# Kernel optimization log

Hardware: AMD Instinct MI355X
Metric: run time of the kernel (lower is better)

Reference implementation:

```python
import jax, jax.numpy as jnp
import numpy as np


def setup_inputs() -> dict:
    key = jax.random.key(0)
    kx, kr, kq, kk, kv = jax.random.split(key, 5)
    B, T, N, C = 4, 8, 2048, 128
    w_scale = 1.0 / np.sqrt(C)  # keep logits in a sane range
    return {
        "x": jax.random.normal(kx, (B, T, N, C), dtype=jnp.float32),
        "residual_source": jax.random.normal(kr, (B, N, C), dtype=jnp.float32),
        "Wq": jax.random.normal(kq, (C, C), dtype=jnp.float32) * w_scale,
        "Wk": jax.random.normal(kk, (C, C), dtype=jnp.float32) * w_scale,
        "Wv": jax.random.normal(kv, (C, C), dtype=jnp.float32) * w_scale,
    }


def reference(x, residual_source, Wq, Wk, Wv):
    # x: [B, T, N, C]; residual_source: [B, M, C] (expanded along T in the
    # original via unsqueeze+expand; here we exploit broadcasting instead of
    # materializing the [B, T, M, C] copy -- same math, k/v identical per T).
    q = jnp.einsum("btnc,cd->btnd", x, Wq)               # [B, T, N, D]
    k = jnp.einsum("bmc,cd->bmd", residual_source, Wk)   # [B, M, D]
    v = jnp.einsum("bmc,cd->bmd", residual_source, Wv)   # [B, M, D]
    # Unscaled attention, exactly as in the original (no 1/sqrt(d)).
    affinities = jnp.einsum("btnd,bmd->btnm", q, k)       # [B, T, N, M]
    attn = jax.nn.softmax(affinities, axis=-1)
    residual = jnp.einsum("btnm,bmd->btnd", attn, v)      # [B, T, N, D]
    return x + residual
```

## Files before the change

kernel.cpp:

```cpp
#include <hip/hip_runtime.h>


#define Bn 4
#define Tn 8
#define Nn 2048
#define Cn 128
#define Mn 2048
#define NTILES 32
#define QROWS 128
#define NQT (Nn / QROWS)

typedef __attribute__((ext_vector_type(4))) float f32x4;
typedef __attribute__((ext_vector_type(16))) float f32x16;
typedef __attribute__((ext_vector_type(8))) _Float16 f16x8;
typedef __attribute__((ext_vector_type(4))) unsigned int u32x4;
typedef __attribute__((address_space(3))) unsigned char lds_uc;
typedef const __attribute__((address_space(1))) unsigned char glb_uc;

__device__ __forceinline__ unsigned short f2h(float f) {
  _Float16 h = (_Float16)f;
  return __builtin_bit_cast(unsigned short, h);
}
__device__ __forceinline__ unsigned int pk2(float a, float b) {
  auto v = __builtin_amdgcn_cvt_pkrtz(a, b);
  return __builtin_bit_cast(unsigned int, v);
}
__device__ __forceinline__ f16x8 lds_read8w(const unsigned char* base, int row,
                                            int colByte) {
  int byte = row * 256 + (colByte ^ ((row & 15) << 4));
  return *(const f16x8*)(base + byte);
}
__device__ __forceinline__ f16x8 lds_read8v(const unsigned char* base, int row,
                                            int colByte) {
  int byte = row * 128 + (colByte ^ ((row & 7) << 4));
  return *(const f16x8*)(base + byte);
}
__device__ __forceinline__ void gld16(const void* g, void* l) {
  __builtin_amdgcn_global_load_lds((glb_uc*)g, (lds_uc*)l, 16, 0, 0);
}

#define MKPF(dst, sv, base)                                        \
  {                                                                \
    unsigned a0 = pk2(sv[base + 0], sv[base + 1]);                 \
    unsigned b0 = pk2(sv[base + 4], sv[base + 5]);                 \
    unsigned a1 = pk2(sv[base + 2], sv[base + 3]);                 \
    unsigned b1 = pk2(sv[base + 6], sv[base + 7]);                 \
    asm("v_permlane32_swap_b32 %0, %1" : "+v"(a0), "+v"(b0));      \
    asm("v_permlane32_swap_b32 %0, %1" : "+v"(a1), "+v"(b1));      \
    u32x4 tmp = {a0, a1, b0, b1};                                  \
    dst = __builtin_bit_cast(f16x8, tmp);                          \
  }

__global__ __launch_bounds__(256) void proj_kv_kernel(
    const float* __restrict__ rs, const float* __restrict__ Wk,
    const float* __restrict__ Wv, unsigned short* __restrict__ k_ws,
    unsigned short* __restrict__ vt_ws) {
  __shared__ unsigned char smem[48 * 1024];
  unsigned char* rsh = smem;
  unsigned char* wt = smem + 16 * 1024;

  const int bid = blockIdx.x;
  const int b = bid >> 5;
  const int kt = bid & 31;
  const int m0 = kt << 6;
  const int tid = threadIdx.x;
  const int wv = tid >> 6, lane = tid & 63;

  {
    const float4* g = (const float4*)(rs + ((size_t)b * Mn + m0) * Cn);
#pragma unroll
    for (int i = 0; i < 8; ++i) {
      int f = tid + i * 256;
      int row = f >> 5, c4 = f & 31;
      float4 v = g[f];
      int byte = row * 256 + ((c4 * 8) ^ ((row & 15) << 4));
      *(ushort4*)(rsh + byte) =
          make_ushort4(f2h(v.x), f2h(v.y), f2h(v.z), f2h(v.w));
    }
  }

#define STAGE_WT(Wp)                                                          \
  {                                                                           \
    const float4* g = (const float4*)(Wp);                                    \
    _Pragma("unroll") for (int i = 0; i < 16; ++i) {                          \
      int f = tid + i * 256;                                                  \
      int cc = f >> 5, d0 = (f & 31) * 4;                                     \
      float4 v = g[f];                                                        \
      float vv[4] = {v.x, v.y, v.z, v.w};                                     \
      _Pragma("unroll") for (int j = 0; j < 4; ++j) {                         \
        int row = d0 + j;                                                     \
        int byte = row * 256 + ((cc * 2) ^ ((row & 15) << 4));                \
        *(unsigned short*)(wt + byte) = f2h(vv[j]);                           \
      }                                                                       \
    }                                                                         \
  }

  STAGE_WT(Wk);
  __syncthreads();

  const int arow = wv * 16 + (lane & 15);
  f16x8 ah[4];
#pragma unroll
  for (int ks = 0; ks < 4; ++ks)
    ah[ks] = lds_read8w(rsh, arow, (lane >> 4) * 16 + ks * 64);

  f32x4 acc[8];
#pragma unroll
  for (int df = 0; df < 8; ++df) acc[df] = (f32x4)(0.0f);
#pragma unroll
  for (int ks = 0; ks < 4; ++ks)
#pragma unroll
    for (int df = 0; df < 8; ++df) {
      f16x8 bf = lds_read8w(wt, df * 16 + (lane & 15), (lane >> 4) * 16 + ks * 64);
      acc[df] = __builtin_amdgcn_mfma_f32_16x16x32_f16(ah[ks], bf, acc[df], 0, 0, 0);
    }
  {
    unsigned char* kb = (unsigned char*)k_ws + ((size_t)b * NTILES + kt) * 16384;
#pragma unroll
    for (int df = 0; df < 8; ++df)
#pragma unroll
      for (int r = 0; r < 4; ++r) {
        int row = wv * 16 + (lane >> 4) * 4 + r;
        int dcol = df * 16 + (lane & 15);
        int byte = row * 256 + ((dcol * 2) ^ ((row & 15) << 4));
        *(unsigned short*)(kb + byte) = f2h(acc[df][r]);
      }
  }
  __syncthreads();

  STAGE_WT(Wv);
  __syncthreads();
#pragma unroll
  for (int df = 0; df < 8; ++df) acc[df] = (f32x4)(0.0f);
#pragma unroll
  for (int ks = 0; ks < 4; ++ks)
#pragma unroll
    for (int df = 0; df < 8; ++df) {
      f16x8 bf = lds_read8w(wt, df * 16 + (lane & 15), (lane >> 4) * 16 + ks * 64);
      acc[df] = __builtin_amdgcn_mfma_f32_16x16x32_f16(ah[ks], bf, acc[df], 0, 0, 0);
    }
  {
    unsigned char* vb = (unsigned char*)vt_ws + ((size_t)b * NTILES + kt) * 16384;
#pragma unroll
    for (int df = 0; df < 8; ++df)
#pragma unroll
      for (int r = 0; r < 4; ++r) {
        int row = wv * 16 + (lane >> 4) * 4 + r;
        int dcol = df * 16 + (lane & 15);
        int byte = dcol * 128 + ((row * 2) ^ ((dcol & 7) << 4));
        *(unsigned short*)(vb + byte) = f2h(acc[df][r]);
      }
  }
#undef STAGE_WT
}

__global__ __launch_bounds__(256, 2) void attn_kernel(
    const float* __restrict__ x, const float* __restrict__ Wq,
    const unsigned short* __restrict__ k_ws,
    const unsigned short* __restrict__ vt_ws, float* __restrict__ out) {
  __shared__ unsigned char smem[64 * 1024];

  const int bx = blockIdx.x;
  const int wb = ((bx & 7) << 6) | (bx >> 3);
  const int b = wb >> 7;
  const int t_ = (wb >> 4) & 7;
  const int n0 = (wb & 15) * QROWS;
  const int tid = threadIdx.x;
  const int wv = tid >> 6, lane = tid & 63;
  const int c = lane & 15, g = lane >> 4;
  const int l31 = lane & 31, hi = lane >> 5;

  const float* xg = x + (((size_t)b * Tn + t_) * Nn + n0) * Cn;
  unsigned char* xa = smem;
  unsigned char* wqb = smem + 32 * 1024;

  const float LOG2E = 1.4426950408889634f;
  {
    const float4* gp = (const float4*)xg;
#pragma unroll
    for (int ii = 0; ii < 16; ++ii) {
      int f = tid + ii * 256;
      int row = f >> 5, c4 = f & 31;
      float4 v = gp[f];
      int byte = row * 256 + ((c4 * 8) ^ ((row & 15) << 4));
      *(ushort4*)(xa + byte) =
          make_ushort4(f2h(v.x), f2h(v.y), f2h(v.z), f2h(v.w));
    }
  }
  {
    const float4* gp = (const float4*)Wq;
#pragma unroll
    for (int ii = 0; ii < 16; ++ii) {
      int f = tid + ii * 256;
      int cc = f >> 5, d0 = (f & 31) * 4;
      float4 v = gp[f];
      float vv[4] = {v.x, v.y, v.z, v.w};
#pragma unroll
      for (int j = 0; j < 4; ++j) {
        int row = d0 + j;
        int byte = row * 256 + ((cc * 2) ^ ((row & 15) << 4));
        *(unsigned short*)(wqb + byte) = f2h(vv[j] * LOG2E);
      }
    }
  }
  __syncthreads();

  {
    f32x4 qacc[2][8];
#pragma unroll
    for (int rb = 0; rb < 2; ++rb)
#pragma unroll
      for (int df = 0; df < 8; ++df) qacc[rb][df] = (f32x4)(0.0f);
    f16x8 xf[2][4];
#pragma unroll
    for (int rb = 0; rb < 2; ++rb)
#pragma unroll
      for (int ks = 0; ks < 4; ++ks)
        xf[rb][ks] = lds_read8w(xa, wv * 32 + rb * 16 + c, g * 16 + ks * 64);
#pragma unroll
    for (int ks = 0; ks < 4; ++ks)
#pragma unroll
      for (int df = 0; df < 8; ++df) {
        f16x8 bf = lds_read8w(wqb, df * 16 + c, g * 16 + ks * 64);
        qacc[0][df] = __builtin_amdgcn_mfma_f32_16x16x32_f16(xf[0][ks], bf, qacc[0][df], 0, 0, 0);
        qacc[1][df] = __builtin_amdgcn_mfma_f32_16x16x32_f16(xf[1][ks], bf, qacc[1][df], 0, 0, 0);
      }
#pragma unroll
    for (int rb = 0; rb < 2; ++rb)
#pragma unroll
      for (int df = 0; df < 8; ++df)
#pragma unroll
        for (int r = 0; r < 4; ++r) {
          int row = wv * 32 + rb * 16 + g * 4 + r;
          int col = df * 16 + c;
          int byte = row * 256 + ((col * 2) ^ ((row & 15) << 4));
          *(unsigned short*)(xa + byte) = f2h(qacc[rb][df][r]);
        }
  }
  f16x8 qf[8];
#pragma unroll
  for (int kc = 0; kc < 8; ++kc)
    qf[kc] = lds_read8w(xa, wv * 32 + l31, kc * 32 + hi * 16);
  __syncthreads();

  f32x16 o[4];
#pragma unroll
  for (int dblk = 0; dblk < 4; ++dblk) o[dblk] = (f32x16)(0.0f);
  float mrow = -INFINITY;
  float lrow = 0.f;

  const unsigned char* khg = (const unsigned char*)k_ws + (size_t)b * NTILES * 16384;
  const unsigned char* vtg = (const unsigned char*)vt_ws + (size_t)b * NTILES * 16384;

  auto stage = [&](int t) {
    unsigned char* kd = smem + (t & 1) * 16384 + tid * 16;
    unsigned char* vd = smem + 32 * 1024 + (t & 1) * 16384 + tid * 16;
    const unsigned char* ksrc = khg + (size_t)t * 16384 + tid * 16;
    const unsigned char* vsrc = vtg + (size_t)t * 16384 + tid * 16;
#pragma unroll
    for (int h = 0; h < 4; ++h) {
      gld16(ksrc + h * 4096, kd + h * 4096);
      gld16(vsrc + h * 4096, vd + h * 4096);
    }
  };

  stage(0);
  __syncthreads();

#pragma unroll 1
  for (int t = 0; t < NTILES; ++t) {
    unsigned char* kb = smem + (t & 1) * 16384;
    unsigned char* vb = smem + 32 * 1024 + (t & 1) * 16384;
    if (t + 1 < NTILES) stage(t + 1);

    f32x16 s0 = (f32x16)(0.0f), s1 = (f32x16)(0.0f);
    __builtin_amdgcn_s_setprio(1);
#pragma unroll
    for (int kc = 0; kc < 8; ++kc) {
      f16x8 kf0 = lds_read8w(kb, l31, kc * 32 + hi * 16);
      f16x8 kf1 = lds_read8w(kb, 32 + l31, kc * 32 + hi * 16);
      s0 = __builtin_amdgcn_mfma_f32_32x32x16_f16(kf0, qf[kc], s0, 0, 0, 0);
      s1 = __builtin_amdgcn_mfma_f32_32x32x16_f16(kf1, qf[kc], s1, 0, 0, 0);
    }
    __builtin_amdgcn_s_setprio(0);

    float tm;
    {
      float mx[16];
#pragma unroll
      for (int r = 0; r < 16; ++r) mx[r] = fmaxf(s0[r], s1[r]);
#pragma unroll
      for (int r = 0; r < 8; ++r) mx[r] = fmaxf(mx[r], mx[r + 8]);
#pragma unroll
      for (int r = 0; r < 4; ++r) mx[r] = fmaxf(mx[r], mx[r + 4]);
      tm = fmaxf(fmaxf(mx[0], mx[1]), fmaxf(mx[2], mx[3]));
    }
    tm = fmaxf(tm, __shfl_xor(tm, 32));
    if (__any(tm > mrow + 8.f)) {
      float newm = fmaxf(mrow, tm);
      float scl = exp2f(mrow - newm);
#pragma unroll
      for (int dblk = 0; dblk < 4; ++dblk) o[dblk] *= scl;
      lrow *= scl;
      mrow = newm;
    }
    {
      float ps = 0.f;
#pragma unroll
      for (int r = 0; r < 16; ++r) {
        float p = exp2f(s0[r] - mrow);
        s0[r] = p;
        ps += p;
      }
#pragma unroll
      for (int r = 0; r < 16; ++r) {
        float p = exp2f(s1[r] - mrow);
        s1[r] = p;
        ps += p;
      }
      lrow += ps;
    }

    f16x8 pf0, pf1, pf2, pf3;
    MKPF(pf0, s0, 0);
    MKPF(pf1, s0, 8);
    MKPF(pf2, s1, 0);
    MKPF(pf3, s1, 8);

    __builtin_amdgcn_s_setprio(1);
#pragma unroll
    for (int dblk = 0; dblk < 4; ++dblk) {
      f16x8 vf0 = lds_read8v(vb, dblk * 32 + l31, 0 * 32 + hi * 16);
      f16x8 vf1 = lds_read8v(vb, dblk * 32 + l31, 1 * 32 + hi * 16);
      f16x8 vf2 = lds_read8v(vb, dblk * 32 + l31, 2 * 32 + hi * 16);
      f16x8 vf3 = lds_read8v(vb, dblk * 32 + l31, 3 * 32 + hi * 16);
      o[dblk] = __builtin_amdgcn_mfma_f32_32x32x16_f16(vf0, pf0, o[dblk], 0, 0, 0);
      o[dblk] = __builtin_amdgcn_mfma_f32_32x32x16_f16(vf1, pf1, o[dblk], 0, 0, 0);
      o[dblk] = __builtin_amdgcn_mfma_f32_32x32x16_f16(vf2, pf2, o[dblk], 0, 0, 0);
      o[dblk] = __builtin_amdgcn_mfma_f32_32x32x16_f16(vf3, pf3, o[dblk], 0, 0, 0);
    }
    __builtin_amdgcn_s_setprio(0);
    __syncthreads();
  }

  lrow += __shfl_xor(lrow, 32);
  float inv = 1.0f / lrow;
#pragma unroll
  for (int dblk = 0; dblk < 4; ++dblk)
#pragma unroll
    for (int rg = 0; rg < 4; ++rg) {
      f32x4 v;
      v[0] = o[dblk][rg * 4 + 0] * inv;
      v[1] = o[dblk][rg * 4 + 1] * inv;
      v[2] = o[dblk][rg * 4 + 2] * inv;
      v[3] = o[dblk][rg * 4 + 3] * inv;
      int row = wv * 32 + l31;
      int colb = dblk * 128 + rg * 32 + hi * 16;
      int byte = row * 512 + (colb ^ ((row & 7) << 4));
      *(f32x4*)(smem + byte) = v;
    }
  __syncthreads();
  {
    const float4* xg4 = (const float4*)xg;
    float4* og4 = (float4*)(out + (((size_t)b * Tn + t_) * Nn + n0) * Cn);
#pragma unroll
    for (int ii = 0; ii < 16; ++ii) {
      int f = tid + ii * 256;
      int row = f >> 5, slot = f & 31;
      int byte = row * 512 + ((slot * 16) ^ ((row & 7) << 4));
      f32x4 v = *(const f32x4*)(smem + byte);
      float4 xv = xg4[f];
      og4[f] = make_float4(xv.x + v[0], xv.y + v[1], xv.z + v[2], xv.w + v[3]);
    }
  }
}

extern "C" void kernel_launch(void* const* d_in, const int* in_sizes, int n_in,
                              void* d_out, int out_size, void* d_ws,
                              size_t ws_size, hipStream_t stream) {
  const float* x = (const float*)d_in[0];
  const float* rs = (const float*)d_in[1];
  const float* Wq = (const float*)d_in[2];
  const float* Wk = (const float*)d_in[3];
  const float* Wv = (const float*)d_in[4];
  float* out = (float*)d_out;

  unsigned short* k_ws = (unsigned short*)d_ws;
  unsigned short* vt_ws = k_ws + (size_t)Bn * Mn * Cn;

  proj_kv_kernel<<<Bn * NTILES, 256, 0, stream>>>(rs, Wk, Wv, k_ws, vt_ws);
  attn_kernel<<<Bn * Tn * NQT, 256, 0, stream>>>(x, Wq, k_ws, vt_ws, out);
}
```

Measured before the change: 121.8 us.

## Split KV tile softmax into two sub-blocks to interleave MFMA and exp

```diff
diff --git a/kernel.cpp b/kernel.cpp
--- a/kernel.cpp
+++ b/kernel.cpp
@@ -264,6 +264,41 @@
     }
   };
 
+  auto softmax_sub = [&](f32x16& s, f16x8& pfA, f16x8& pfB) {
+    float mx[8];
+#pragma unroll
+    for (int r = 0; r < 8; ++r) mx[r] = fmaxf(s[r], s[r + 8]);
+#pragma unroll
+    for (int r = 0; r < 4; ++r) mx[r] = fmaxf(mx[r], mx[r + 4]);
+    float tm = fmaxf(fmaxf(mx[0], mx[1]), fmaxf(mx[2], mx[3]));
+    tm = fmaxf(tm, __shfl_xor(tm, 32));
+    if (__any(tm > mrow + 8.f)) {
+      float newm = fmaxf(mrow, tm);
+      float scl = __builtin_amdgcn_exp2f(mrow - newm);
+#pragma unroll
+      for (int dblk = 0; dblk < 4; ++dblk) o[dblk] *= scl;
+      lrow *= scl;
+      mrow = newm;
+    }
+    float p[16];
+#pragma unroll
+    for (int r = 0; r < 16; ++r) p[r] = __builtin_amdgcn_exp2f(s[r] - mrow);
+    float ps = 0.f;
+    {
+      float a[8];
+#pragma unroll
+      for (int r = 0; r < 8; ++r) a[r] = p[r] + p[r + 8];
+#pragma unroll
+      for (int r = 0; r < 4; ++r) a[r] += a[r + 4];
+      ps = (a[0] + a[1]) + (a[2] + a[3]);
+    }
+    lrow += ps;
+#pragma unroll
+    for (int r = 0; r < 16; ++r) s[r] = p[r];
+    MKPF(pfA, s, 0);
+    MKPF(pfB, s, 8);
+  };
+
   stage(0);
   __syncthreads();
 
@@ -271,71 +306,48 @@
   for (int t = 0; t < NTILES; ++t) {
     unsigned char* kb = smem + (t & 1) * 16384;
     unsigned char* vb = smem + 32 * 1024 + (t & 1) * 16384;
-    if (t + 1 < NTILES) stage(t + 1);
-
-    f32x16 s0 = (f32x16)(0.0f), s1 = (f32x16)(0.0f);
+
+    f32x16 s0 = (f32x16)(0.0f);
     __builtin_amdgcn_s_setprio(1);
 #pragma unroll
     for (int kc = 0; kc < 8; ++kc) {
       f16x8 kf0 = lds_read8w(kb, l31, kc * 32 + hi * 16);
+      s0 = __builtin_amdgcn_mfma_f32_32x32x16_f16(kf0, qf[kc], s0, 0, 0, 0);
+    }
+    __builtin_amdgcn_s_setprio(0);
+
+    if (t + 1 < NTILES) stage(t + 1);
+
+    f32x16 s1 = (f32x16)(0.0f);
+    __builtin_amdgcn_s_setprio(1);
+#pragma unroll
+    for (int kc = 0; kc < 8; ++kc) {
       f16x8 kf1 = lds_read8w(kb, 32 + l31, kc * 32 + hi * 16);
-      s0 = __builtin_amdgcn_mfma_f32_32x32x16_f16(kf0, qf[kc], s0, 0, 0, 0);
       s1 = __builtin_amdgcn_mfma_f32_32x32x16_f16(kf1, qf[kc], s1, 0, 0, 0);
     }
     __builtin_amdgcn_s_setprio(0);
 
-    float tm;
-    {
-      float mx[16];
-#pragma unroll
-      for (int r = 0; r < 16; ++r) mx[r] = fmaxf(s0[r], s1[r]);
-#pragma unroll
-      for (int r = 0; r < 8; ++r) mx[r] = fmaxf(mx[r], mx[r + 8]);
-#pragma unroll
-      for (int r = 0; r < 4; ++r) mx[r] = fmaxf(mx[r], mx[r + 4]);
-      tm = fmaxf(fmaxf(mx[0], mx[1]), fmaxf(mx[2], mx[3]));
-    }
-    tm = fmaxf(tm, __shfl_xor(tm, 32));
-    if (__any(tm > mrow + 8.f)) {
-      float newm = fmaxf(mrow, tm);
-      float scl = exp2f(mrow - newm);
-#pragma unroll
-      for (int dblk = 0; dblk < 4; ++dblk) o[dblk] *= scl;
-      lrow *= scl;
-      mrow = newm;
-    }
-    {
-      float ps = 0.f;
-#pragma unroll
-      for (int r = 0; r < 16; ++r) {
-        float p = exp2f(s0[r] - mrow);
-        s0[r] = p;
-        ps += p;
-      }
-#pragma unroll
-      for (int r = 0; r < 16; ++r) {
-        float p = exp2f(s1[r] - mrow);
-        s1[r] = p;
-        ps += p;
-      }
-      lrow += ps;
-    }
-
-    f16x8 pf0, pf1, pf2, pf3;
-    MKPF(pf0, s0, 0);
-    MKPF(pf1, s0, 8);
-    MKPF(pf2, s1, 0);
-    MKPF(pf3, s1, 8);
+    f16x8 pf0, pf1;
+    softmax_sub(s0, pf0, pf1);
 
     __builtin_amdgcn_s_setprio(1);
 #pragma unroll
     for (int dblk = 0; dblk < 4; ++dblk) {
       f16x8 vf0 = lds_read8v(vb, dblk * 32 + l31, 0 * 32 + hi * 16);
       f16x8 vf1 = lds_read8v(vb, dblk * 32 + l31, 1 * 32 + hi * 16);
+      o[dblk] = __builtin_amdgcn_mfma_f32_32x32x16_f16(vf0, pf0, o[dblk], 0, 0, 0);
+      o[dblk] = __builtin_amdgcn_mfma_f32_32x32x16_f16(vf1, pf1, o[dblk], 0, 0, 0);
+    }
+    __builtin_amdgcn_s_setprio(0);
+
+    f16x8 pf2, pf3;
+    softmax_sub(s1, pf2, pf3);
+
+    __builtin_amdgcn_s_setprio(1);
+#pragma unroll
+    for (int dblk = 0; dblk < 4; ++dblk) {
       f16x8 vf2 = lds_read8v(vb, dblk * 32 + l31, 2 * 32 + hi * 16);
       f16x8 vf3 = lds_read8v(vb, dblk * 32 + l31, 3 * 32 + hi * 16);
-      o[dblk] = __builtin_amdgcn_mfma_f32_32x32x16_f16(vf0, pf0, o[dblk], 0, 0, 0);
-      o[dblk] = __builtin_amdgcn_mfma_f32_32x32x16_f16(vf1, pf1, o[dblk], 0, 0, 0);
       o[dblk] = __builtin_amdgcn_mfma_f32_32x32x16_f16(vf2, pf2, o[dblk], 0, 0, 0);
       o[dblk] = __builtin_amdgcn_mfma_f32_32x32x16_f16(vf3, pf3, o[dblk], 0, 0, 0);
     }
```

Measured after the change: 109.7 us. 1.11x faster.
